# Optimization experiments

Hardware: AMD Instinct MI355X
Metric: run time of the kernel (lower is better)

The kernel has to match this reference:

```python
import jax, jax.numpy as jnp
import numpy as np

B, NORB, N_UP, N_DN, HIDDEN = 1024, 128, 32, 32, 4096


def setup_inputs() -> dict:
    rng = np.random.default_rng(0)
    # Build valid occupancy configs: exactly N_UP up-electrons (bit 0) and
    # N_DN down-electrons (bit 1) per sample. Encoding: 0=empty,1=up,2=dn,3=updn.
    up_order = np.argsort(rng.random((B, NORB)), axis=1)
    dn_order = np.argsort(rng.random((B, NORB)), axis=1)
    up_bit = np.zeros((B, NORB), np.int32)
    dn_bit = np.zeros((B, NORB), np.int32)
    np.put_along_axis(up_bit, up_order[:, :N_UP], 1, axis=1)
    np.put_along_axis(dn_bit, dn_order[:, :N_DN], 1, axis=1)
    x = jnp.asarray(up_bit + 2 * dn_bit, dtype=jnp.int32)

    key = jax.random.key(0)
    k1, k2, k3 = jax.random.split(key, 3)
    orbitals = jax.random.normal(k1, (NORB, N_UP), jnp.float32)
    W1 = jax.random.normal(k2, (4 * NORB, HIDDEN), jnp.float32) / np.sqrt(4 * NORB)
    b1 = jnp.zeros((HIDDEN,), jnp.float32)
    W2 = jax.random.normal(k3, (HIDDEN, NORB * N_UP), jnp.float32) / np.sqrt(HIDDEN)
    b2 = jnp.zeros((NORB * N_UP,), jnp.float32)
    return {"x": x, "orbitals": orbitals, "W1": W1, "b1": b1, "W2": W2, "b2": b2}


def _occupancies_to_electrons(x, n_up, n_dn):
    # Per-spin sorted positions of occupied orbitals. Stable argsort on the
    # inverted mask keeps occupied sites first, in ascending orbital order.
    up_mask = (x & 1) == 1
    dn_mask = (x & 2) == 2
    y_up = jnp.argsort(jnp.where(up_mask, 0, 1), axis=-1, stable=True)[:, :n_up]
    y_dn = jnp.argsort(jnp.where(dn_mask, 0, 1), axis=-1, stable=True)[:, :n_dn]
    return y_up, y_dn


def reference(x, orbitals, W1, b1, W2, b2):
    Bsz, norb = x.shape
    n_up = orbitals.shape[1]

    # correction_fun: MLP on one-hot config -> [B, norb, n_up]
    h = jax.nn.one_hot(x, 4, dtype=W1.dtype).reshape(Bsz, -1)  # [B, 4*norb]
    h = jax.nn.relu(h @ W1 + b1)                               # [B, hidden]
    corrections = (h @ W2 + b2).reshape(Bsz, norb, n_up)       # [B, norb, n_up]

    y_up, y_dn = _occupancies_to_electrons(x, n_up, n_up)
    y_up = y_up[..., None]  # [B, n_up, 1]
    y_dn = y_dn[..., None]

    # gather orbital rows + correction rows per electron (spin-symmetric orbitals)
    phi_up = jnp.take_along_axis(orbitals[None], y_up, axis=1)  # [B, n_up, n_up]
    phi_dn = jnp.take_along_axis(orbitals[None], y_dn, axis=1)
    d_up = jnp.take_along_axis(corrections, y_up, axis=1)
    d_dn = jnp.take_along_axis(corrections, y_dn, axis=1)

    s_up, log_det_up = jnp.linalg.slogdet(phi_up + d_up)
    s_dn, log_det_dn = jnp.linalg.slogdet(phi_dn + d_dn)
    return log_det_up + log_det_dn + jnp.log(s_up * s_dn + 0j)  # complex [B]
```

## Files before the change

### kernel.cpp

```cpp
#include <hip/hip_runtime.h>
#include <cmath>

#define B_SZ  1024
#define NORB  128
#define NUP   32
#define HID   4096
#define NCORR (NORB * NUP)
#define K1    (4 * NORB)

typedef short    bf16x8 __attribute__((ext_vector_type(8)));
typedef _Float16 f16x8  __attribute__((ext_vector_type(8)));
typedef float    f32x4  __attribute__((ext_vector_type(4)));

__device__ __forceinline__ unsigned short f2bf_rne(float f) {
    unsigned int u = __float_as_uint(f);
    u += 0x7FFFu + ((u >> 16) & 1u);
    return (unsigned short)(u >> 16);
}

__global__ __launch_bounds__(256) void k_splitW(const float* __restrict__ W,
                                                unsigned short* __restrict__ Bph,
                                                unsigned short* __restrict__ Bpl,
                                                int ktTot) {
    __shared__ float tile[64][33];
    int n0 = blockIdx.x * 32, k0 = blockIdx.y * 64;
    int t = threadIdx.x;

    int rl = t >> 3, c4 = (t & 7) * 4;
#pragma unroll
    for (int i = 0; i < 2; ++i) {
        int kl = rl + 32 * i;
        float4 v = *(const float4*)(W + (size_t)(k0 + kl) * 4096 + n0 + c4);
        tile[kl][c4 + 0] = v.x; tile[kl][c4 + 1] = v.y;
        tile[kl][c4 + 2] = v.z; tile[kl][c4 + 3] = v.w;
    }
    __syncthreads();

    int nl = t & 31, kg = t >> 5;
    int nt = (n0 + nl) >> 4;
    int kt = (k0 >> 5) + (kg >> 2);
    int lane_o = (kg & 3) * 16 + (nl & 15);
    size_t o = (((size_t)nt * ktTot + kt) * 64 + lane_o) * 8;

    unsigned short hi8[8], lo8[8];
#pragma unroll
    for (int j = 0; j < 8; ++j) {
        float v = tile[kg * 8 + j][nl];
        unsigned short hi = f2bf_rne(v);
        float fhi = __uint_as_float((unsigned int)hi << 16);
        hi8[j] = hi;
        lo8[j] = f2bf_rne(v - fhi);
    }
    *(bf16x8*)(Bph + o) = *(bf16x8*)hi8;
    *(bf16x8*)(Bpl + o) = *(bf16x8*)lo8;
}

__global__ __launch_bounds__(256) void k_splitW16(const float* __restrict__ W,
                                                  _Float16* __restrict__ Bph,
                                                  _Float16* __restrict__ Bpl) {
    __shared__ float tile[64][33];
    int n0 = blockIdx.x * 32, k0 = blockIdx.y * 64;
    int t = threadIdx.x;

    int rl = t >> 3, c4 = (t & 7) * 4;
#pragma unroll
    for (int i = 0; i < 2; ++i) {
        int kl = rl + 32 * i;
        float4 v = *(const float4*)(W + (size_t)(k0 + kl) * 4096 + n0 + c4);
        tile[kl][c4 + 0] = v.x; tile[kl][c4 + 1] = v.y;
        tile[kl][c4 + 2] = v.z; tile[kl][c4 + 3] = v.w;
    }
    __syncthreads();

    int nl = t & 31, kg = t >> 5;
    int nt = (n0 + nl) >> 4;
    int kt = (k0 >> 5) + (kg >> 2);
    int lane_o = (kg & 3) * 16 + (nl & 15);
    size_t o = (((size_t)nt * 128 + kt) * 64 + lane_o) * 8;

    f16x8 hi8, lo8;
#pragma unroll
    for (int j = 0; j < 8; ++j) {
        float v = tile[kg * 8 + j][nl];
        _Float16 hi = (_Float16)v;
        hi8[j] = hi;
        lo8[j] = (_Float16)((v - (float)hi) * 2048.0f);
    }
    *(f16x8*)(Bph + o) = hi8;
    *(f16x8*)(Bpl + o) = lo8;
}

__global__ __launch_bounds__(256, 2) void k_hidden3(const int* __restrict__ x,
                                                    const unsigned short* __restrict__ Bph,
                                                    const unsigned short* __restrict__ Bpl,
                                                    const float* __restrict__ b1,
                                                    _Float16* __restrict__ h16) {
    __shared__ unsigned int sxp[64][8];
    __shared__ unsigned short BF[2][4][4][512];
    __shared__ float Ht[64][132];

    int n0 = blockIdx.x * 128;
    int m0 = blockIdx.y * 64;
    int t = threadIdx.x;
    int w = t >> 6, lane = t & 63;
    int lm = lane & 15, kq = lane >> 4;
    int wn = w * 32;

#pragma unroll
    for (int i = 0; i < 2; ++i) {
        int id = t + 256 * i;
        int row = id >> 3, d = id & 7;
        const int* src = x + (size_t)(m0 + row) * NORB + d * 16;
        unsigned int dw = 0;
#pragma unroll
        for (int b = 0; b < 16; ++b) dw |= ((unsigned int)(src[b] & 3)) << (2 * b);
        sxp[row][d] = dw;
    }

    int nt0 = (n0 + wn) >> 4;
    const unsigned short* bh0 = Bph + (size_t)nt0 * (16 * 512) + (size_t)lane * 8;
    const unsigned short* bh1 = Bph + (size_t)(nt0 + 1) * (16 * 512) + (size_t)lane * 8;
    const unsigned short* bl0 = Bpl + (size_t)nt0 * (16 * 512) + (size_t)lane * 8;
    const unsigned short* bl1 = Bpl + (size_t)(nt0 + 1) * (16 * 512) + (size_t)lane * 8;

    f32x4 acc[4][2] = {};

    bf16x8 r0 = *(const bf16x8*)(bh0);
    bf16x8 r1 = *(const bf16x8*)(bh1);
    bf16x8 r2 = *(const bf16x8*)(bl0);
    bf16x8 r3 = *(const bf16x8*)(bl1);
    bf16x8 r4 = *(const bf16x8*)(bh0 + 512);
    bf16x8 r5 = *(const bf16x8*)(bh1 + 512);
    bf16x8 r6 = *(const bf16x8*)(bl0 + 512);
    bf16x8 r7 = *(const bf16x8*)(bl1 + 512);

    __syncthreads();

    for (int p = 0; p < 8; ++p) {
        if (p) __syncthreads();

        *(bf16x8*)&BF[0][w][0][lane * 8] = r0;
        *(bf16x8*)&BF[0][w][1][lane * 8] = r1;
        *(bf16x8*)&BF[0][w][2][lane * 8] = r2;
        *(bf16x8*)&BF[0][w][3][lane * 8] = r3;
        *(bf16x8*)&BF[1][w][0][lane * 8] = r4;
        *(bf16x8*)&BF[1][w][1][lane * 8] = r5;
        *(bf16x8*)&BF[1][w][2][lane * 8] = r6;
        *(bf16x8*)&BF[1][w][3][lane * 8] = r7;
        __syncthreads();

        int kn = (p + 1 < 8) ? p + 1 : 7;
        r0 = *(const bf16x8*)(bh0 + (2 * kn) * 512);
        r1 = *(const bf16x8*)(bh1 + (2 * kn) * 512);
        r2 = *(const bf16x8*)(bl0 + (2 * kn) * 512);
        r3 = *(const bf16x8*)(bl1 + (2 * kn) * 512);
        r4 = *(const bf16x8*)(bh0 + (2 * kn + 1) * 512);
        r5 = *(const bf16x8*)(bh1 + (2 * kn + 1) * 512);
        r6 = *(const bf16x8*)(bl0 + (2 * kn + 1) * 512);
        r7 = *(const bf16x8*)(bl1 + (2 * kn + 1) * 512);
        __builtin_amdgcn_sched_barrier(0);

#pragma unroll
        for (int s = 0; s < 2; ++s) {
            int kt = 2 * p + s;
            int i0 = kt * 8 + kq * 2;
            int dwIdx = i0 >> 4;
            int sh = (i0 & 15) * 2;
            bf16x8 af[4];
#pragma unroll
            for (int fm = 0; fm < 4; ++fm) {
                unsigned int dw = sxp[fm * 16 + lm][dwIdx];
                unsigned int c01 = (dw >> sh) & 0xFu;
                union { bf16x8 v; unsigned long long u[2]; } a;
                a.u[0] = 0x3F80ULL << ((c01 & 3u) * 16);
                a.u[1] = 0x3F80ULL << ((c01 >> 2) * 16);
                af[fm] = a.v;
            }

            bf16x8 b0h = *(const bf16x8*)&BF[s][w][0][lane * 8];
            bf16x8 b1h = *(const bf16x8*)&BF[s][w][1][lane * 8];
            bf16x8 b0l = *(const bf16x8*)&BF[s][w][2][lane * 8];
            bf16x8 b1l = *(const bf16x8*)&BF[s][w][3][lane * 8];

#pragma unroll
            for (int fm = 0; fm < 4; ++fm) {
                acc[fm][0] = __builtin_amdgcn_mfma_f32_16x16x32_bf16(af[fm], b0h, acc[fm][0], 0, 0, 0);
                acc[fm][0] = __builtin_amdgcn_mfma_f32_16x16x32_bf16(af[fm], b0l, acc[fm][0], 0, 0, 0);
                acc[fm][1] = __builtin_amdgcn_mfma_f32_16x16x32_bf16(af[fm], b1h, acc[fm][1], 0, 0, 0);
                acc[fm][1] = __builtin_amdgcn_mfma_f32_16x16x32_bf16(af[fm], b1l, acc[fm][1], 0, 0, 0);
            }
        }
    }

    __syncthreads();
#pragma unroll
    for (int fm = 0; fm < 4; ++fm)
#pragma unroll
        for (int fn = 0; fn < 2; ++fn) {
            int n = wn + fn * 16 + lm;
            float bv = b1[n0 + n];
#pragma unroll
            for (int r = 0; r < 4; ++r)
                Ht[fm * 16 + kq * 4 + r][n] = fmaxf(acc[fm][fn][r] + bv, 0.f);
        }
    __syncthreads();

    size_t mt0 = (size_t)(m0 >> 4), kt0 = (size_t)(n0 >> 5);
#pragma unroll
    for (int fi = 0; fi < 4; ++fi) {
        int f = w * 4 + fi;
        int mt = f >> 2, ktn = f & 3;
        int m = mt * 16 + lm;
        int kn = ktn * 32 + kq * 8;
        float4 v0 = *(const float4*)&Ht[m][kn];
        float4 v1 = *(const float4*)&Ht[m][kn + 4];
        float vv[8] = {v0.x, v0.y, v0.z, v0.w, v1.x, v1.y, v1.z, v1.w};
        f16x8 o16;
#pragma unroll
        for (int j = 0; j < 8; ++j) o16[j] = (_Float16)vv[j];
        size_t o = (((mt0 + mt) * 128 + (kt0 + ktn)) * 64 + lane) * 8;
        *(f16x8*)(h16 + o) = o16;
    }
}

__global__ __launch_bounds__(256) void k_hidden_f32(const int* __restrict__ x,
                                                    const float* __restrict__ W1,
                                                    const float* __restrict__ b1,
                                                    float* __restrict__ h) {
    int b = blockIdx.x, tid = threadIdx.x;
    __shared__ int sx[NORB];
    if (tid < NORB) sx[tid] = x[b * NORB + tid];
    __syncthreads();
    float acc[16];
#pragma unroll
    for (int u = 0; u < 16; ++u) acc[u] = b1[tid + 256 * u];
    for (int i = 0; i < NORB; ++i) {
        const float* row = W1 + (size_t)(4 * i + sx[i]) * HID;
#pragma unroll
        for (int u = 0; u < 16; ++u) acc[u] += row[tid + 256 * u];
    }
    float* hb = h + (size_t)b * HID;
#pragma unroll
    for (int u = 0; u < 16; ++u) hb[tid + 256 * u] = fmaxf(acc[u], 0.f);
}

__global__ __launch_bounds__(256, 2) void k_gemm7(const _Float16* __restrict__ Ap,
                                                  const _Float16* __restrict__ Bph,
                                                  const _Float16* __restrict__ Bpl,
                                                  const float* __restrict__ bias,
                                                  float* __restrict__ C) {
    __shared__ _Float16 AF[2][2][4][512];

    int n0 = blockIdx.x * 128;
    int m0 = blockIdx.y * 64;
    int t = threadIdx.x;
    int w = t >> 6, lane = t & 63;
    int lm = lane & 15, kq = lane >> 4;
    int wn = w * 32;

    int mt0 = m0 >> 4;
    int nt0 = (n0 + wn) >> 4;

    const _Float16* ag  = Ap  + (size_t)(mt0 + w) * 65536 + (size_t)lane * 8;
    const _Float16* bh0 = Bph + (size_t)nt0 * 65536 + (size_t)lane * 8;
    const _Float16* bh1 = Bph + (size_t)(nt0 + 1) * 65536 + (size_t)lane * 8;
    const _Float16* bl0 = Bpl + (size_t)nt0 * 65536 + (size_t)lane * 8;
    const _Float16* bl1 = Bpl + (size_t)(nt0 + 1) * 65536 + (size_t)lane * 8;

    f32x4 accH[4][2] = {}, accL[4][2] = {};

    f16x8 r0 = *(const f16x8*)(ag);
    f16x8 r1 = *(const f16x8*)(ag + 512);
    f16x8 B0h0 = *(const f16x8*)(bh0);
    f16x8 B0h1 = *(const f16x8*)(bh1);
    f16x8 B0l0 = *(const f16x8*)(bl0);
    f16x8 B0l1 = *(const f16x8*)(bl1);
    f16x8 B1h0 = *(const f16x8*)(bh0 + 512);
    f16x8 B1h1 = *(const f16x8*)(bh1 + 512);
    f16x8 B1l0 = *(const f16x8*)(bl0 + 512);
    f16x8 B1l1 = *(const f16x8*)(bl1 + 512);

    for (int ktp = 0; ktp < 64; ++ktp) {
        int buf = ktp & 1;
        *(f16x8*)&AF[buf][0][w][lane * 8] = r0;
        *(f16x8*)&AF[buf][1][w][lane * 8] = r1;
        __syncthreads();

        int kn = (ktp + 1 < 64) ? ktp + 1 : 63;
        size_t o0 = (size_t)(2 * kn) * 512, o1 = o0 + 512;
        f16x8 nr0 = *(const f16x8*)(ag + o0);
        f16x8 nr1 = *(const f16x8*)(ag + o1);
        f16x8 nB0h0 = *(const f16x8*)(bh0 + o0);
        f16x8 nB0h1 = *(const f16x8*)(bh1 + o0);
        f16x8 nB0l0 = *(const f16x8*)(bl0 + o0);
        f16x8 nB0l1 = *(const f16x8*)(bl1 + o0);
        f16x8 nB1h0 = *(const f16x8*)(bh0 + o1);
        f16x8 nB1h1 = *(const f16x8*)(bh1 + o1);
        f16x8 nB1l0 = *(const f16x8*)(bl0 + o1);
        f16x8 nB1l1 = *(const f16x8*)(bl1 + o1);
        __builtin_amdgcn_sched_barrier(0);

        f16x8 a0[4], a1[4];
#pragma unroll
        for (int fm = 0; fm < 4; ++fm) {
            a0[fm] = *(const f16x8*)&AF[buf][0][fm][lane * 8];
            a1[fm] = *(const f16x8*)&AF[buf][1][fm][lane * 8];
        }

#pragma unroll
        for (int fm = 0; fm < 4; ++fm) {
            accH[fm][0] = __builtin_amdgcn_mfma_f32_16x16x32_f16(a0[fm], B0h0, accH[fm][0], 0, 0, 0);
            accL[fm][0] = __builtin_amdgcn_mfma_f32_16x16x32_f16(a0[fm], B0l0, accL[fm][0], 0, 0, 0);
            accH[fm][1] = __builtin_amdgcn_mfma_f32_16x16x32_f16(a0[fm], B0h1, accH[fm][1], 0, 0, 0);
            accL[fm][1] = __builtin_amdgcn_mfma_f32_16x16x32_f16(a0[fm], B0l1, accL[fm][1], 0, 0, 0);
        }
#pragma unroll
        for (int fm = 0; fm < 4; ++fm) {
            accH[fm][0] = __builtin_amdgcn_mfma_f32_16x16x32_f16(a1[fm], B1h0, accH[fm][0], 0, 0, 0);
            accL[fm][0] = __builtin_amdgcn_mfma_f32_16x16x32_f16(a1[fm], B1l0, accL[fm][0], 0, 0, 0);
            accH[fm][1] = __builtin_amdgcn_mfma_f32_16x16x32_f16(a1[fm], B1h1, accH[fm][1], 0, 0, 0);
            accL[fm][1] = __builtin_amdgcn_mfma_f32_16x16x32_f16(a1[fm], B1l1, accL[fm][1], 0, 0, 0);
        }

        r0 = nr0; r1 = nr1;
        B0h0 = nB0h0; B0h1 = nB0h1; B0l0 = nB0l0; B0l1 = nB0l1;
        B1h0 = nB1h0; B1h1 = nB1h1; B1l0 = nB1l0; B1l1 = nB1l1;
    }

    const float ls = 1.0f / 2048.0f;
#pragma unroll
    for (int fm = 0; fm < 4; ++fm)
#pragma unroll
        for (int fn = 0; fn < 2; ++fn) {
            int n = n0 + wn + fn * 16 + lm;
            float bv = bias[n];
#pragma unroll
            for (int r = 0; r < 4; ++r) {
                int m = m0 + fm * 16 + kq * 4 + r;
                C[(size_t)m * NCORR + n] = accH[fm][fn][r] + ls * accL[fm][fn][r] + bv;
            }
        }
}

#define BM 64
#define BN 64
#define BK 32
__global__ __launch_bounds__(256) void k_gemm(const float* __restrict__ A,
                                              const float* __restrict__ Bm,
                                              const float* __restrict__ bias,
                                              float* __restrict__ C) {
    __shared__ float As[BK][68];
    __shared__ float Bs[BK][BN];
    int n0 = blockIdx.x * BN, m0 = blockIdx.y * BM;
    int tid = threadIdx.x;
    int tm = tid >> 4, tn = tid & 15;
    int am = tid >> 3, ak = (tid & 7) * 4;
    int bk = tid >> 4, bn = (tid & 15) * 4;
    float acc[4][4] = {};
    for (int k0 = 0; k0 < HID; k0 += BK) {
#pragma unroll
        for (int s = 0; s < 2; ++s) {
            int m = am + 32 * s;
            float4 v = *(const float4*)(A + (size_t)(m0 + m) * HID + k0 + ak);
            As[ak + 0][m] = v.x; As[ak + 1][m] = v.y;
            As[ak + 2][m] = v.z; As[ak + 3][m] = v.w;
        }
#pragma unroll
        for (int s = 0; s < 2; ++s) {
            int k = bk + 16 * s;
            float4 v = *(const float4*)(Bm + (size_t)(k0 + k) * NCORR + n0 + bn);
            *(float4*)&Bs[k][bn] = v;
        }
        __syncthreads();
#pragma unroll
        for (int kk = 0; kk < BK; ++kk) {
            float4 a = *(const float4*)&As[kk][tm * 4];
            float4 bv = *(const float4*)&Bs[kk][tn * 4];
            float av[4] = {a.x, a.y, a.z, a.w};
            float bb[4] = {bv.x, bv.y, bv.z, bv.w};
#pragma unroll
            for (int i = 0; i < 4; ++i)
#pragma unroll
                for (int j = 0; j < 4; ++j) acc[i][j] += av[i] * bb[j];
        }
        __syncthreads();
    }
#pragma unroll
    for (int i = 0; i < 4; ++i) {
        int m = m0 + tm * 4 + i;
        float4 o;
        o.x = acc[i][0] + bias[n0 + tn * 4 + 0];
        o.y = acc[i][1] + bias[n0 + tn * 4 + 1];
        o.z = acc[i][2] + bias[n0 + tn * 4 + 2];
        o.w = acc[i][3] + bias[n0 + tn * 4 + 3];
        *(float4*)(C + (size_t)m * NCORR + n0 + tn * 4) = o;
    }
}

__global__ __launch_bounds__(128) void k_det(const int* __restrict__ x,
                                             const float* __restrict__ orbitals,
                                             const float* __restrict__ corr,
                                             float* __restrict__ out,
                                             int imag_off) {
    int b = blockIdx.x, tid = threadIdx.x;
    __shared__ int sx[NORB];
    __shared__ int yup[NUP], ydn[NUP];
    __shared__ float M[2][NUP][NUP + 1];
    __shared__ float rlog[2];
    __shared__ int rneg[2];

    sx[tid] = x[b * NORB + tid];
    __syncthreads();

    int occ = sx[tid];
    if (occ & 1) {
        int r = 0;
        for (int i = 0; i < tid; ++i) r += sx[i] & 1;
        yup[r] = tid;
    }
    if (occ & 2) {
        int r = 0;
        for (int i = 0; i < tid; ++i) r += (sx[i] >> 1) & 1;
        ydn[r] = tid;
    }
    __syncthreads();

    const float* cb = corr + (size_t)b * NCORR;
    for (int idx = tid; idx < 2 * NUP * NUP; idx += 128) {
        int s = idx >> 10;
        int i = (idx >> 5) & 31;
        int j = idx & 31;
        int r = s ? ydn[i] : yup[i];
        M[s][i][j] = orbitals[r * NUP + j] + cb[r * NUP + j];
    }
    __syncthreads();

    int wv = tid >> 6, lane = tid & 63;
    float (*Mm)[NUP + 1] = M[wv];
    float logdet = 0.f;
    int neg = 0;

    for (int k = 0; k < NUP; ++k) {
        float v = (lane >= k && lane < NUP) ? fabsf(Mm[lane][k]) : -1.f;
        int pi = lane;
#pragma unroll
        for (int off = 32; off > 0; off >>= 1) {
            float v2 = __shfl_down(v, off);
            int p2 = __shfl_down(pi, off);
            if (v2 > v) { v = v2; pi = p2; }
        }
        int p = __shfl(pi, 0);

        if (p != k) {
            if (lane < NUP) {
                float t1 = Mm[k][lane];
                Mm[k][lane] = Mm[p][lane];
                Mm[p][lane] = t1;
            }
            neg ^= 1;
        }
        __syncthreads();

        float pv = Mm[k][k];
        logdet += logf(fabsf(pv));
        if (pv < 0.f) neg ^= 1;

        int row = k + 1 + (lane & 31);
        int half = lane >> 5;
        if (row < NUP) {
            float f = Mm[row][k] / pv;
            for (int j = k + 1 + half; j < NUP; j += 2)
                Mm[row][j] -= f * Mm[k][j];
        }
        __syncthreads();
    }

    if (lane == 0) { rlog[wv] = logdet; rneg[wv] = neg; }
    __syncthreads();
    if (tid == 0) {
        out[b] = rlog[0] + rlog[1];
        if (imag_off > 0)
            out[imag_off + b] =
                (rneg[0] ^ rneg[1]) ? 3.14159265358979323846f : 0.f;
    }
}

extern "C" void kernel_launch(void* const* d_in, const int* in_sizes, int n_in,
                              void* d_out, int out_size, void* d_ws, size_t ws_size,
                              hipStream_t stream) {
    const int*   x        = (const int*)d_in[0];
    const float* orbitals = (const float*)d_in[1];
    const float* W1       = (const float*)d_in[2];
    const float* b1       = (const float*)d_in[3];
    const float* W2       = (const float*)d_in[4];
    const float* b2       = (const float*)d_in[5];
    float* out = (float*)d_out;
    int imag_off = (out_size == 2 * B_SZ) ? B_SZ : 0;

    const size_t need = (size_t)96 * 1024 * 1024;
    if (ws_size >= need) {
        _Float16* h16  = (_Float16*)d_ws;
        _Float16* Bh16 = h16 + (size_t)B_SZ * HID;
        _Float16* Bl16 = Bh16 + (size_t)HID * NCORR;
        float*    corr = (float*)(Bl16 + (size_t)HID * NCORR);

        unsigned short* W1ph = (unsigned short*)corr;
        unsigned short* W1pl = W1ph + (size_t)K1 * HID;

        k_splitW<<<dim3(HID / 32, K1 / 64), 256, 0, stream>>>(W1, W1ph, W1pl, 16);
        k_splitW16<<<dim3(NCORR / 32, HID / 64), 256, 0, stream>>>(W2, Bh16, Bl16);

        k_hidden3<<<dim3(HID / 128, B_SZ / 64), 256, 0, stream>>>(x, W1ph, W1pl, b1, h16);

        dim3 g2(NCORR / 128, B_SZ / 64);
        k_gemm7<<<g2, 256, 0, stream>>>(h16, Bh16, Bl16, b2, corr);
        k_det<<<B_SZ, 128, 0, stream>>>(x, orbitals, corr, out, imag_off);
    } else {
        float* h    = (float*)d_ws;
        float* corr = h + (size_t)B_SZ * HID;
        k_hidden_f32<<<B_SZ, 256, 0, stream>>>(x, W1, b1, h);
        dim3 g2(NCORR / BN, B_SZ / BM);
        k_gemm<<<g2, 256, 0, stream>>>(h, W2, b2, corr);
        k_det<<<B_SZ, 128, 0, stream>>>(x, orbitals, corr, out, imag_off);
    }
}
```

Before: 241.0 us.

## Fuse W2 fp16 hi/lo split into GEMM B-operand loading

```diff
diff --git a/kernel.cpp b/kernel.cpp
--- a/kernel.cpp
+++ b/kernel.cpp
@@ -53,41 +53,6 @@
     }
     *(bf16x8*)(Bph + o) = *(bf16x8*)hi8;
     *(bf16x8*)(Bpl + o) = *(bf16x8*)lo8;
-}
-
-__global__ __launch_bounds__(256) void k_splitW16(const float* __restrict__ W,
-                                                  _Float16* __restrict__ Bph,
-                                                  _Float16* __restrict__ Bpl) {
-    __shared__ float tile[64][33];
-    int n0 = blockIdx.x * 32, k0 = blockIdx.y * 64;
-    int t = threadIdx.x;
-
-    int rl = t >> 3, c4 = (t & 7) * 4;
-#pragma unroll
-    for (int i = 0; i < 2; ++i) {
-        int kl = rl + 32 * i;
-        float4 v = *(const float4*)(W + (size_t)(k0 + kl) * 4096 + n0 + c4);
-        tile[kl][c4 + 0] = v.x; tile[kl][c4 + 1] = v.y;
-        tile[kl][c4 + 2] = v.z; tile[kl][c4 + 3] = v.w;
-    }
-    __syncthreads();
-
-    int nl = t & 31, kg = t >> 5;
-    int nt = (n0 + nl) >> 4;
-    int kt = (k0 >> 5) + (kg >> 2);
-    int lane_o = (kg & 3) * 16 + (nl & 15);
-    size_t o = (((size_t)nt * 128 + kt) * 64 + lane_o) * 8;
-
-    f16x8 hi8, lo8;
-#pragma unroll
-    for (int j = 0; j < 8; ++j) {
-        float v = tile[kg * 8 + j][nl];
-        _Float16 hi = (_Float16)v;
-        hi8[j] = hi;
-        lo8[j] = (_Float16)((v - (float)hi) * 2048.0f);
-    }
-    *(f16x8*)(Bph + o) = hi8;
-    *(f16x8*)(Bpl + o) = lo8;
 }
 
 __global__ __launch_bounds__(256, 2) void k_hidden3(const int* __restrict__ x,
@@ -244,11 +209,10 @@
     for (int u = 0; u < 16; ++u) hb[tid + 256 * u] = fmaxf(acc[u], 0.f);
 }
 
-__global__ __launch_bounds__(256, 2) void k_gemm7(const _Float16* __restrict__ Ap,
-                                                  const _Float16* __restrict__ Bph,
-                                                  const _Float16* __restrict__ Bpl,
-                                                  const float* __restrict__ bias,
-                                                  float* __restrict__ C) {
+__global__ __launch_bounds__(256, 2) void k_gemm10(const _Float16* __restrict__ Ap,
+                                                   const float* __restrict__ W2f,
+                                                   const float* __restrict__ bias,
+                                                   float* __restrict__ C) {
     __shared__ _Float16 AF[2][2][4][512];
 
     int n0 = blockIdx.x * 128;
@@ -261,24 +225,21 @@
     int mt0 = m0 >> 4;
     int nt0 = (n0 + wn) >> 4;
 
-    const _Float16* ag  = Ap  + (size_t)(mt0 + w) * 65536 + (size_t)lane * 8;
-    const _Float16* bh0 = Bph + (size_t)nt0 * 65536 + (size_t)lane * 8;
-    const _Float16* bh1 = Bph + (size_t)(nt0 + 1) * 65536 + (size_t)lane * 8;
-    const _Float16* bl0 = Bpl + (size_t)nt0 * 65536 + (size_t)lane * 8;
-    const _Float16* bl1 = Bpl + (size_t)(nt0 + 1) * 65536 + (size_t)lane * 8;
+    const _Float16* ag = Ap + (size_t)(mt0 + w) * 65536 + (size_t)lane * 8;
+    const float* bW = W2f + (size_t)(kq * 8) * 4096 + (size_t)nt0 * 16 + lm;
 
     f32x4 accH[4][2] = {}, accL[4][2] = {};
 
     f16x8 r0 = *(const f16x8*)(ag);
     f16x8 r1 = *(const f16x8*)(ag + 512);
-    f16x8 B0h0 = *(const f16x8*)(bh0);
-    f16x8 B0h1 = *(const f16x8*)(bh1);
-    f16x8 B0l0 = *(const f16x8*)(bl0);
-    f16x8 B0l1 = *(const f16x8*)(bl1);
-    f16x8 B1h0 = *(const f16x8*)(bh0 + 512);
-    f16x8 B1h1 = *(const f16x8*)(bh1 + 512);
-    f16x8 B1l0 = *(const f16x8*)(bl0 + 512);
-    f16x8 B1l1 = *(const f16x8*)(bl1 + 512);
+    float cB[4][8];
+#pragma unroll
+    for (int s = 0; s < 2; ++s)
+#pragma unroll
+        for (int c = 0; c < 2; ++c)
+#pragma unroll
+            for (int j = 0; j < 8; ++j)
+                cB[s * 2 + c][j] = bW[(size_t)(s * 32 + j) * 4096 + c * 16];
 
     for (int ktp = 0; ktp < 64; ++ktp) {
         int buf = ktp & 1;
@@ -287,17 +248,17 @@
         __syncthreads();
 
         int kn = (ktp + 1 < 64) ? ktp + 1 : 63;
-        size_t o0 = (size_t)(2 * kn) * 512, o1 = o0 + 512;
-        f16x8 nr0 = *(const f16x8*)(ag + o0);
-        f16x8 nr1 = *(const f16x8*)(ag + o1);
-        f16x8 nB0h0 = *(const f16x8*)(bh0 + o0);
-        f16x8 nB0h1 = *(const f16x8*)(bh1 + o0);
-        f16x8 nB0l0 = *(const f16x8*)(bl0 + o0);
-        f16x8 nB0l1 = *(const f16x8*)(bl1 + o0);
-        f16x8 nB1h0 = *(const f16x8*)(bh0 + o1);
-        f16x8 nB1h1 = *(const f16x8*)(bh1 + o1);
-        f16x8 nB1l0 = *(const f16x8*)(bl0 + o1);
-        f16x8 nB1l1 = *(const f16x8*)(bl1 + o1);
+        f16x8 nr0 = *(const f16x8*)(ag + (size_t)(2 * kn) * 512);
+        f16x8 nr1 = *(const f16x8*)(ag + (size_t)(2 * kn + 1) * 512);
+        float nB[4][8];
+#pragma unroll
+        for (int s = 0; s < 2; ++s)
+#pragma unroll
+            for (int c = 0; c < 2; ++c)
+#pragma unroll
+                for (int j = 0; j < 8; ++j)
+                    nB[s * 2 + c][j] =
+                        bW[(size_t)((2 * kn + s) * 32 + j) * 4096 + c * 16];
         __builtin_amdgcn_sched_barrier(0);
 
         f16x8 a0[4], a1[4];
@@ -308,23 +269,34 @@
         }
 
 #pragma unroll
-        for (int fm = 0; fm < 4; ++fm) {
-            accH[fm][0] = __builtin_amdgcn_mfma_f32_16x16x32_f16(a0[fm], B0h0, accH[fm][0], 0, 0, 0);
-            accL[fm][0] = __builtin_amdgcn_mfma_f32_16x16x32_f16(a0[fm], B0l0, accL[fm][0], 0, 0, 0);
-            accH[fm][1] = __builtin_amdgcn_mfma_f32_16x16x32_f16(a0[fm], B0h1, accH[fm][1], 0, 0, 0);
-            accL[fm][1] = __builtin_amdgcn_mfma_f32_16x16x32_f16(a0[fm], B0l1, accL[fm][1], 0, 0, 0);
-        }
-#pragma unroll
-        for (int fm = 0; fm < 4; ++fm) {
-            accH[fm][0] = __builtin_amdgcn_mfma_f32_16x16x32_f16(a1[fm], B1h0, accH[fm][0], 0, 0, 0);
-            accL[fm][0] = __builtin_amdgcn_mfma_f32_16x16x32_f16(a1[fm], B1l0, accL[fm][0], 0, 0, 0);
-            accH[fm][1] = __builtin_amdgcn_mfma_f32_16x16x32_f16(a1[fm], B1h1, accH[fm][1], 0, 0, 0);
-            accL[fm][1] = __builtin_amdgcn_mfma_f32_16x16x32_f16(a1[fm], B1l1, accL[fm][1], 0, 0, 0);
+        for (int s = 0; s < 2; ++s) {
+            f16x8 bh0, bl0, bh1, bl1;
+#pragma unroll
+            for (int j = 0; j < 8; ++j) {
+                float v0 = cB[s * 2 + 0][j];
+                _Float16 h0 = (_Float16)v0;
+                bh0[j] = h0;
+                bl0[j] = (_Float16)((v0 - (float)h0) * 2048.0f);
+                float v1 = cB[s * 2 + 1][j];
+                _Float16 h1 = (_Float16)v1;
+                bh1[j] = h1;
+                bl1[j] = (_Float16)((v1 - (float)h1) * 2048.0f);
+            }
+#pragma unroll
+            for (int fm = 0; fm < 4; ++fm) {
+                f16x8 a = s ? a1[fm] : a0[fm];
+                accH[fm][0] = __builtin_amdgcn_mfma_f32_16x16x32_f16(a, bh0, accH[fm][0], 0, 0, 0);
+                accL[fm][0] = __builtin_amdgcn_mfma_f32_16x16x32_f16(a, bl0, accL[fm][0], 0, 0, 0);
+                accH[fm][1] = __builtin_amdgcn_mfma_f32_16x16x32_f16(a, bh1, accH[fm][1], 0, 0, 0);
+                accL[fm][1] = __builtin_amdgcn_mfma_f32_16x16x32_f16(a, bl1, accL[fm][1], 0, 0, 0);
+            }
         }
 
         r0 = nr0; r1 = nr1;
-        B0h0 = nB0h0; B0h1 = nB0h1; B0l0 = nB0l0; B0l1 = nB0l1;
-        B1h0 = nB1h0; B1h1 = nB1h1; B1l0 = nB1l0; B1l1 = nB1l1;
+#pragma unroll
+        for (int f = 0; f < 4; ++f)
+#pragma unroll
+            for (int j = 0; j < 8; ++j) cB[f][j] = nB[f][j];
     }
 
     const float ls = 1.0f / 2048.0f;
@@ -497,23 +469,21 @@
     float* out = (float*)d_out;
     int imag_off = (out_size == 2 * B_SZ) ? B_SZ : 0;
 
-    const size_t need = (size_t)96 * 1024 * 1024;
+    const size_t need = (size_t)32 * 1024 * 1024;
     if (ws_size >= need) {
         _Float16* h16  = (_Float16*)d_ws;
-        _Float16* Bh16 = h16 + (size_t)B_SZ * HID;
-        _Float16* Bl16 = Bh16 + (size_t)HID * NCORR;
-        float*    corr = (float*)(Bl16 + (size_t)HID * NCORR);
+        float*    corr = (float*)(h16 + (size_t)B_SZ * HID);
 
         unsigned short* W1ph = (unsigned short*)corr;
         unsigned short* W1pl = W1ph + (size_t)K1 * HID;
 
         k_splitW<<<dim3(HID / 32, K1 / 64), 256, 0, stream>>>(W1, W1ph, W1pl, 16);
-        k_splitW16<<<dim3(NCORR / 32, HID / 64), 256, 0, stream>>>(W2, Bh16, Bl16);
 
         k_hidden3<<<dim3(HID / 128, B_SZ / 64), 256, 0, stream>>>(x, W1ph, W1pl, b1, h16);
 
         dim3 g2(NCORR / 128, B_SZ / 64);
-        k_gemm7<<<g2, 256, 0, stream>>>(h16, Bh16, Bl16, b2, corr);
+        k_gemm10<<<g2, 256, 0, stream>>>(h16, W2, b2, corr);
+
         k_det<<<B_SZ, 128, 0, stream>>>(x, orbitals, corr, out, imag_off);
     } else {
         float* h    = (float*)d_ws;
```

New measurement: 245.1 us. About the same (+1.7%).
